# Kernel optimization log

Measured on AMD Instinct MI355X. Metric: run time of the kernel, lower is better.

## Reference

```python
import jax, jax.numpy as jnp
import numpy as np

HEADS = 16
DIM_HEAD = 64
DIM = 1024
DIM_HIDDEN = HEADS * DIM_HEAD


def setup_inputs() -> dict:
    key = jax.random.key(0)
    ks = jax.random.split(key, 5)
    b, n = 4, 2048
    x = jax.random.normal(ks[0], (b, n, DIM), dtype=jnp.float32)
    # nn.Linear weights stored as [out, in]; init ~ U(-1/sqrt(in), 1/sqrt(in))
    s = 1.0 / np.sqrt(DIM)
    w_q = jax.random.uniform(ks[1], (DIM_HIDDEN, DIM), minval=-s, maxval=s, dtype=jnp.float32)
    w_kv = jax.random.uniform(ks[2], (2 * DIM_HIDDEN, DIM), minval=-s, maxval=s, dtype=jnp.float32)
    so = 1.0 / np.sqrt(DIM_HIDDEN)
    w_out = jax.random.uniform(ks[3], (DIM, DIM_HIDDEN), minval=-so, maxval=so, dtype=jnp.float32)
    b_out = jax.random.uniform(ks[4], (DIM,), minval=-so, maxval=so, dtype=jnp.float32)
    return {"x": x, "w_q": w_q, "w_kv": w_kv, "w_out": w_out, "b_out": b_out}


def reference(x, w_q, w_kv, w_out, b_out):
    b, n, _ = x.shape
    h, e = HEADS, DIM_HEAD
    q = x @ w_q.T                     # [b, n, h*e]
    kv = x @ w_kv.T                   # [b, n, 2*h*e]
    k, v = jnp.split(kv, 2, axis=-1)
    split = lambda t: t.reshape(b, n, h, e).transpose(0, 2, 1, 3)  # [b, h, n, e]
    q, k, v = split(q), split(k), split(v)
    scale = e ** (-0.5)
    energy = jnp.einsum('bhie,bhje->bhij', q, k) * scale
    attn_w = jax.nn.softmax(energy, axis=-1)
    attn = jnp.einsum('bhij,bhje->bhie', attn_w, v)  # [b, h, n, e]
    out = attn.transpose(0, 2, 1, 3).reshape(b, n, h * e)
    return out @ w_out.T + b_out
```

## Files before the change

kernel.cpp:

```cpp
#include <hip/hip_runtime.h>

typedef __attribute__((ext_vector_type(8))) short bf16x8;
typedef __attribute__((ext_vector_type(4))) float f32x4;

#define AS1 __attribute__((address_space(1)))
#define AS3 __attribute__((address_space(3)))

#if defined(__has_builtin)
#  if __has_builtin(__builtin_amdgcn_exp2f)
#    define EXP2F(x) __builtin_amdgcn_exp2f(x)
#  endif
#endif
#ifndef EXP2F
#  define EXP2F(x) __builtin_exp2f(x)
#endif

__device__ __forceinline__ unsigned short f2bf(float f) {
    union { float f; unsigned u; } v; v.f = f;
    unsigned r = v.u + 0x7fffu + ((v.u >> 16) & 1u);
    return (unsigned short)(r >> 16);
}

__device__ __forceinline__ void dma16(const void* g, void* l) {
    __builtin_amdgcn_global_load_lds((const AS1 unsigned int*)g,
                                     (AS3 unsigned int*)l, 16, 0, 0);
}

__global__ __launch_bounds__(256) void convert_regions(
    const float* __restrict__ s0, unsigned short* __restrict__ d0, int n0, float c0,
    const float* __restrict__ s1, unsigned short* __restrict__ d1, int n1, float c1,
    const float* __restrict__ s2, unsigned short* __restrict__ d2, int n2, float c2)
{
    long long e = ((long long)blockIdx.x * 256 + threadIdx.x) * 8;
    const float* s; unsigned short* d; float sc;
    if (e < n0) { s = s0; d = d0; sc = c0; }
    else { e -= n0;
    if (e < n1) { s = s1; d = d1; sc = c1; }
    else { e -= n1;
    if (e < n2) { s = s2; d = d2; sc = c2; } else return; } }
    const float4 f0 = *(const float4*)(s + e);
    const float4 f1 = *(const float4*)(s + e + 4);
    union { unsigned short u[8]; uint4 q; } t;
    t.u[0]=f2bf(f0.x*sc); t.u[1]=f2bf(f0.y*sc); t.u[2]=f2bf(f0.z*sc); t.u[3]=f2bf(f0.w*sc);
    t.u[4]=f2bf(f1.x*sc); t.u[5]=f2bf(f1.y*sc); t.u[6]=f2bf(f1.z*sc); t.u[7]=f2bf(f1.w*sc);
    *(uint4*)(d + e) = t.q;
}

template<int CM>
__global__ __launch_bounds__(256) void gemm128(
    const unsigned short* __restrict__ A, const unsigned short* __restrict__ B,
    void* __restrict__ C0, void* __restrict__ C1, void* __restrict__ C2,
    const float* __restrict__ bias, int M, int N, int K)
{
    __shared__ __align__(16) unsigned short As[128 * 64];
    __shared__ __align__(16) unsigned short Bs[128 * 64];

    const int tid  = threadIdx.x;
    const int wq   = tid >> 6;
    const int lane = tid & 63;
    const int l16  = lane & 15;
    const int quad = lane >> 4;
    const int m0   = blockIdx.x * 128;
    const int n0   = blockIdx.y * 128;
    const int lr   = lane >> 3;
    const int cs   = lane & 7;
    const bool vswap = (CM == 1) && (n0 >= 2048);

    f32x4 acc[4][4];
#pragma unroll
    for (int mt = 0; mt < 4; ++mt)
#pragma unroll
        for (int nt = 0; nt < 4; ++nt) acc[mt][nt] = (f32x4){0.f, 0.f, 0.f, 0.f};

    for (int kk = 0; kk < K; kk += 64) {
        __syncthreads();
#pragma unroll
        for (int i = 0; i < 4; ++i) {
            const int rr = (wq * 4 + i) * 8 + lr;
            const int cg = cs ^ (rr & 7);
            dma16(A + (size_t)(m0 + rr) * K + kk + cg * 8, As + (wq * 4 + i) * 512);
            dma16(B + (size_t)(n0 + rr) * K + kk + cg * 8, Bs + (wq * 4 + i) * 512);
        }
        __syncthreads();

#pragma unroll
        for (int ch = 0; ch < 2; ++ch) {
            const int swz = (((ch * 4 + quad) ^ (l16 & 7)) * 8);
            bf16x8 aF[4], bF[4];
#pragma unroll
            for (int mt = 0; mt < 4; ++mt)
                aF[mt] = *(const bf16x8*)(As + ((wq >> 1) * 64 + mt * 16 + l16) * 64 + swz);
#pragma unroll
            for (int nt = 0; nt < 4; ++nt)
                bF[nt] = *(const bf16x8*)(Bs + ((wq & 1) * 64 + nt * 16 + l16) * 64 + swz);
            if (vswap) {
#pragma unroll
                for (int mt = 0; mt < 4; ++mt)
#pragma unroll
                    for (int nt = 0; nt < 4; ++nt)
                        acc[mt][nt] = __builtin_amdgcn_mfma_f32_16x16x32_bf16(
                            bF[nt], aF[mt], acc[mt][nt], 0, 0, 0);
            } else {
#pragma unroll
                for (int mt = 0; mt < 4; ++mt)
#pragma unroll
                    for (int nt = 0; nt < 4; ++nt)
                        acc[mt][nt] = __builtin_amdgcn_mfma_f32_16x16x32_bf16(
                            aF[mt], bF[nt], acc[mt][nt], 0, 0, 0);
            }
        }
    }

    const int wr = wq >> 1, wc = wq & 1;
    if (CM == 0) {
#pragma unroll
        for (int mt = 0; mt < 4; ++mt)
#pragma unroll
        for (int nt = 0; nt < 4; ++nt) {
            const int coln = n0 + wc * 64 + nt * 16 + l16;
            const float bv = bias ? bias[coln] : 0.f;
#pragma unroll
            for (int r = 0; r < 4; ++r) {
                const int rowm = m0 + wr * 64 + mt * 16 + quad * 4 + r;
                ((float*)C0)[(size_t)rowm * N + coln] = acc[mt][nt][r] + bv;
            }
        }
    } else if (!vswap) {
#pragma unroll
        for (int mt = 0; mt < 4; ++mt)
#pragma unroll
        for (int nt = 0; nt < 4; ++nt) {
            const int coln = n0 + wc * 64 + nt * 16 + l16;
            unsigned short* dst = (coln < 1024) ? (unsigned short*)C0 : (unsigned short*)C1;
            const int h = (coln >> 6) & 15, e = coln & 63;
#pragma unroll
            for (int r = 0; r < 4; ++r) {
                const int rowm = m0 + wr * 64 + mt * 16 + quad * 4 + r;
                const int b = rowm >> 11, n = rowm & 2047;
                dst[(((size_t)(b * 16 + h) * 2048 + n) << 6) + e] = f2bf(acc[mt][nt][r]);
            }
        }
    } else {
#pragma unroll
        for (int mt = 0; mt < 4; ++mt)
#pragma unroll
        for (int nt = 0; nt < 4; ++nt) {
#pragma unroll
            for (int r = 0; r < 4; ++r) {
                const int eg = n0 + wc * 64 + nt * 16 + quad * 4 + r;
                const int h = (eg >> 6) - 32, e = eg & 63;
                const int rowm = m0 + wr * 64 + mt * 16 + l16;
                const int b = rowm >> 11, n = rowm & 2047;
                ((unsigned short*)C2)[((size_t)(b * 16 + h) * 64 + e) * 2048 + n] =
                    f2bf(acc[mt][nt][r]);
            }
        }
    }
}

__global__ __launch_bounds__(256, 2) void attn_kernel(
    const unsigned short* __restrict__ Q, const unsigned short* __restrict__ K,
    const unsigned short* __restrict__ V, unsigned short* __restrict__ O)
{
    __shared__ __align__(16) unsigned short Ks[64 * 64];
    __shared__ __align__(16) unsigned short Vt[64 * 64];
    __shared__ __align__(16) unsigned short Ps[4 * 64 * 72];

    const int tid  = threadIdx.x;
    const int q0   = blockIdx.x * 256;
    const int bh   = blockIdx.y;
    const int wq   = tid >> 6;
    const int lane = tid & 63;
    const int l16  = lane & 15;
    const int quad = lane >> 4;
    const int lr   = lane >> 3;
    const int cs   = lane & 7;

    const unsigned short* Qg = Q + (size_t)bh * 2048 * 64;
    const unsigned short* Kg = K + (size_t)bh * 2048 * 64;
    const unsigned short* Vg = V + (size_t)bh * 64 * 2048;

    bf16x8 bQ[4][2];
#pragma unroll
    for (int sub = 0; sub < 4; ++sub)
#pragma unroll
        for (int ch = 0; ch < 2; ++ch)
            bQ[sub][ch] = *(const bf16x8*)(Qg + (size_t)(q0 + wq * 64 + sub * 16 + l16) * 64
                                           + ch * 32 + quad * 8);

    bf16x8 ones;
#pragma unroll
    for (int i = 0; i < 8; ++i) ones[i] = (short)0x3F80;

    f32x4 o[4][4], lf[4];
#pragma unroll
    for (int s = 0; s < 4; ++s) {
        lf[s] = (f32x4){0.f, 0.f, 0.f, 0.f};
#pragma unroll
        for (int e = 0; e < 4; ++e) o[s][e] = (f32x4){0.f, 0.f, 0.f, 0.f};
    }

    unsigned short* Psw = Ps + wq * 64 * 72;

    for (int kt = 0; kt < 32; ++kt) {
        const int key0 = kt * 64;
        __syncthreads();
#pragma unroll
        for (int i = 0; i < 4; ++i) {
            const int j  = wq * 4 + i;
            const int rr = (j & 7) * 8 + lr;
            const int cg = cs ^ (rr & 7);
            if (j < 8)
                dma16(Kg + (size_t)(key0 + rr) * 64 + cg * 8, Ks + (j & 7) * 512);
            else
                dma16(Vg + (size_t)rr * 2048 + key0 + cg * 8, Vt + (j & 7) * 512);
        }
        __syncthreads();

        f32x4 s[4][4];
#pragma unroll
        for (int sub = 0; sub < 4; ++sub)
#pragma unroll
            for (int c = 0; c < 4; ++c) s[sub][c] = (f32x4){0.f, 0.f, 0.f, 0.f};
#pragma unroll
        for (int ch = 0; ch < 2; ++ch) {
            const int swz = ((ch * 4 + quad) ^ (l16 & 7)) * 8;
#pragma unroll
            for (int c = 0; c < 4; ++c) {
                const bf16x8 aK = *(const bf16x8*)(Ks + (c * 16 + l16) * 64 + swz);
#pragma unroll
                for (int sub = 0; sub < 4; ++sub)
                    s[sub][c] = __builtin_amdgcn_mfma_f32_16x16x32_bf16(
                        aK, bQ[sub][ch], s[sub][c], 0, 0, 0);
            }
        }

#pragma unroll
        for (int sub = 0; sub < 4; ++sub) {
#pragma unroll
            for (int c = 0; c < 4; ++c) {
                const float p0 = EXP2F(s[sub][c][0]);
                const float p1 = EXP2F(s[sub][c][1]);
                const float p2 = EXP2F(s[sub][c][2]);
                const float p3 = EXP2F(s[sub][c][3]);
                uint2 pk;
                pk.x = __builtin_amdgcn_perm(__float_as_uint(p1), __float_as_uint(p0), 0x07060302);
                pk.y = __builtin_amdgcn_perm(__float_as_uint(p3), __float_as_uint(p2), 0x07060302);
                *(uint2*)(Psw + (sub * 16 + l16) * 72 + c * 16 + quad * 4) = pk;
            }
        }

#pragma unroll
        for (int cc = 0; cc < 2; ++cc) {
            const int swz = ((cc * 4 + quad) ^ (l16 & 7)) * 8;
            bf16x8 aP[4];
#pragma unroll
            for (int sub = 0; sub < 4; ++sub) {
                aP[sub] = *(const bf16x8*)(Psw + (sub * 16 + l16) * 72 + cc * 32 + quad * 8);
                lf[sub] = __builtin_amdgcn_mfma_f32_16x16x32_bf16(aP[sub], ones, lf[sub], 0, 0, 0);
            }
#pragma unroll
            for (int et = 0; et < 4; ++et) {
                const bf16x8 bV = *(const bf16x8*)(Vt + (et * 16 + l16) * 64 + swz);
#pragma unroll
                for (int sub = 0; sub < 4; ++sub)
                    o[sub][et] = __builtin_amdgcn_mfma_f32_16x16x32_bf16(
                        aP[sub], bV, o[sub][et], 0, 0, 0);
            }
        }
    }

    const int bb = bh >> 4, hh = bh & 15;
#pragma unroll
    for (int sub = 0; sub < 4; ++sub) {
#pragma unroll
        for (int r = 0; r < 4; ++r) {
            const float linv = 1.0f / lf[sub][r];
            const int qrow = q0 + wq * 64 + sub * 16 + quad * 4 + r;
#pragma unroll
            for (int et = 0; et < 4; ++et) {
                O[(size_t)(bb * 2048 + qrow) * 1024 + hh * 64 + et * 16 + l16] =
                    f2bf(o[sub][et][r] * linv);
            }
        }
    }
}

extern "C" void kernel_launch(void* const* d_in, const int* in_sizes, int n_in,
                              void* d_out, int out_size, void* d_ws, size_t ws_size,
                              hipStream_t stream) {
    const float* x     = (const float*)d_in[0];
    const float* w_q   = (const float*)d_in[1];
    const float* w_kv  = (const float*)d_in[2];
    const float* w_out = (const float*)d_in[3];
    const float* b_out = (const float*)d_in[4];
    const float CEXP = 0.125f * 1.44269504f;
    const size_t MB = 1024 * 1024;

    unsigned short* Qw    = (unsigned short*)d_ws;
    unsigned short* Kw    = (unsigned short*)((char*)d_ws + 16 * MB);
    unsigned short* Vw    = (unsigned short*)((char*)d_ws + 32 * MB);
    unsigned short* Ow    = (unsigned short*)((char*)d_ws + 48 * MB);
    unsigned short* xb    = (unsigned short*)d_out;
    unsigned short* wqkvb = (unsigned short*)((char*)d_out + 16 * MB);
    unsigned short* wob   = Qw;

    convert_regions<<<5632, 256, 0, stream>>>(
        x, xb, 8388608, 1.0f,
        w_q, wqkvb, 1048576, CEXP,
        w_kv, wqkvb + (size_t)1048576, 2097152, 1.0f);

    gemm128<1><<<dim3(64, 24), 256, 0, stream>>>(
        xb, wqkvb, Qw, Kw, Vw, nullptr, 8192, 3072, 1024);

    attn_kernel<<<dim3(8, 64), 256, 0, stream>>>(Qw, Kw, Vw, Ow);

    convert_regions<<<512, 256, 0, stream>>>(
        w_out, wob, 1048576, 1.0f,
        nullptr, nullptr, 0, 0.f, nullptr, nullptr, 0, 0.f);

    gemm128<0><<<dim3(64, 8), 256, 0, stream>>>(
        Ow, wob, d_out, nullptr, nullptr, b_out, 8192, 1024, 1024);
}
```

Before: 298.9 us.

## Double-buffer LDS tiles in GEMM and attention with async prefetch

Both the projection GEMM and the attention kernel now keep two LDS buffers and issue the global-to-LDS DMA for the next tile before computing on the current one. Hand-written waitcnt-plus-barrier sequences (partial vmcnt) replace the two __syncthreads per iteration, so load latency can overlap MFMA work. The cost is doubled LDS for the staging buffers, which may reduce occupancy, especially in the attention kernel. It also depends on the vmcnt values matching the number of outstanding DMA instructions.

```diff
diff --git a/kernel.cpp b/kernel.cpp
--- a/kernel.cpp
+++ b/kernel.cpp
@@ -14,6 +14,11 @@
 #ifndef EXP2F
 #  define EXP2F(x) __builtin_exp2f(x)
 #endif
+
+#define BAR_WAIT_VM8  asm volatile("s_waitcnt vmcnt(8)\ns_barrier" ::: "memory")
+#define BAR_WAIT_VM4  asm volatile("s_waitcnt vmcnt(4)\ns_barrier" ::: "memory")
+#define BAR_WAIT_VM0  asm volatile("s_waitcnt vmcnt(0)\ns_barrier" ::: "memory")
+#define BAR_WAIT_LGKM asm volatile("s_waitcnt lgkmcnt(0)\ns_barrier" ::: "memory")
 
 __device__ __forceinline__ unsigned short f2bf(float f) {
     union { float f; unsigned u; } v; v.f = f;
@@ -52,8 +57,7 @@
     void* __restrict__ C0, void* __restrict__ C1, void* __restrict__ C2,
     const float* __restrict__ bias, int M, int N, int K)
 {
-    __shared__ __align__(16) unsigned short As[128 * 64];
-    __shared__ __align__(16) unsigned short Bs[128 * 64];
+    __shared__ __align__(16) unsigned short smem[2 * 16384];
 
     const int tid  = threadIdx.x;
     const int wq   = tid >> 6;
@@ -72,27 +76,41 @@
 #pragma unroll
         for (int nt = 0; nt < 4; ++nt) acc[mt][nt] = (f32x4){0.f, 0.f, 0.f, 0.f};
 
-    for (int kk = 0; kk < K; kk += 64) {
-        __syncthreads();
+    auto issue = [&](int buf, int kk) {
+        unsigned short* as = smem + buf * 16384;
+        unsigned short* bs = as + 8192;
 #pragma unroll
         for (int i = 0; i < 4; ++i) {
             const int rr = (wq * 4 + i) * 8 + lr;
             const int cg = cs ^ (rr & 7);
-            dma16(A + (size_t)(m0 + rr) * K + kk + cg * 8, As + (wq * 4 + i) * 512);
-            dma16(B + (size_t)(n0 + rr) * K + kk + cg * 8, Bs + (wq * 4 + i) * 512);
-        }
-        __syncthreads();
-
+            dma16(A + (size_t)(m0 + rr) * K + kk + cg * 8, as + (wq * 4 + i) * 512);
+            dma16(B + (size_t)(n0 + rr) * K + kk + cg * 8, bs + (wq * 4 + i) * 512);
+        }
+    };
+
+    const int nIt = K >> 6;
+    issue(0, 0);
+#pragma unroll 2
+    for (int it = 0; it < nIt; ++it) {
+        const int cur = it & 1;
+        if (it + 1 < nIt) {
+            issue(cur ^ 1, (it + 1) << 6);
+            BAR_WAIT_VM8;
+        } else {
+            BAR_WAIT_VM0;
+        }
+        const unsigned short* as = smem + cur * 16384;
+        const unsigned short* bs = as + 8192;
 #pragma unroll
         for (int ch = 0; ch < 2; ++ch) {
             const int swz = (((ch * 4 + quad) ^ (l16 & 7)) * 8);
             bf16x8 aF[4], bF[4];
 #pragma unroll
             for (int mt = 0; mt < 4; ++mt)
-                aF[mt] = *(const bf16x8*)(As + ((wq >> 1) * 64 + mt * 16 + l16) * 64 + swz);
+                aF[mt] = *(const bf16x8*)(as + ((wq >> 1) * 64 + mt * 16 + l16) * 64 + swz);
 #pragma unroll
             for (int nt = 0; nt < 4; ++nt)
-                bF[nt] = *(const bf16x8*)(Bs + ((wq & 1) * 64 + nt * 16 + l16) * 64 + swz);
+                bF[nt] = *(const bf16x8*)(bs + ((wq & 1) * 64 + nt * 16 + l16) * 64 + swz);
             if (vswap) {
 #pragma unroll
                 for (int mt = 0; mt < 4; ++mt)
@@ -109,6 +127,7 @@
                             aF[mt], bF[nt], acc[mt][nt], 0, 0, 0);
             }
         }
+        BAR_WAIT_LGKM;
     }
 
     const int wr = wq >> 1, wc = wq & 1;
@@ -162,8 +181,7 @@
     const unsigned short* __restrict__ Q, const unsigned short* __restrict__ K,
     const unsigned short* __restrict__ V, unsigned short* __restrict__ O)
 {
-    __shared__ __align__(16) unsigned short Ks[64 * 64];
-    __shared__ __align__(16) unsigned short Vt[64 * 64];
+    __shared__ __align__(16) unsigned short KVs[2 * 8192];
     __shared__ __align__(16) unsigned short Ps[4 * 64 * 72];
 
     const int tid  = threadIdx.x;
@@ -202,20 +220,33 @@
 
     unsigned short* Psw = Ps + wq * 64 * 72;
 
-    for (int kt = 0; kt < 32; ++kt) {
-        const int key0 = kt * 64;
-        __syncthreads();
+    auto issueKV = [&](int buf, int key0) {
+        unsigned short* ks = KVs + buf * 8192;
+        unsigned short* vt = ks + 4096;
 #pragma unroll
         for (int i = 0; i < 4; ++i) {
             const int j  = wq * 4 + i;
             const int rr = (j & 7) * 8 + lr;
             const int cg = cs ^ (rr & 7);
             if (j < 8)
-                dma16(Kg + (size_t)(key0 + rr) * 64 + cg * 8, Ks + (j & 7) * 512);
+                dma16(Kg + (size_t)(key0 + rr) * 64 + cg * 8, ks + (j & 7) * 512);
             else
-                dma16(Vg + (size_t)rr * 2048 + key0 + cg * 8, Vt + (j & 7) * 512);
-        }
-        __syncthreads();
+                dma16(Vg + (size_t)rr * 2048 + key0 + cg * 8, vt + (j & 7) * 512);
+        }
+    };
+
+    issueKV(0, 0);
+#pragma unroll 2
+    for (int kt = 0; kt < 32; ++kt) {
+        const int cur = kt & 1;
+        if (kt + 1 < 32) {
+            issueKV(cur ^ 1, (kt + 1) * 64);
+            BAR_WAIT_VM4;
+        } else {
+            BAR_WAIT_VM0;
+        }
+        const unsigned short* ks = KVs + cur * 8192;
+        const unsigned short* vt = ks + 4096;
 
         f32x4 s[4][4];
 #pragma unroll
@@ -227,7 +258,7 @@
             const int swz = ((ch * 4 + quad) ^ (l16 & 7)) * 8;
 #pragma unroll
             for (int c = 0; c < 4; ++c) {
-                const bf16x8 aK = *(const bf16x8*)(Ks + (c * 16 + l16) * 64 + swz);
+                const bf16x8 aK = *(const bf16x8*)(ks + (c * 16 + l16) * 64 + swz);
 #pragma unroll
                 for (int sub = 0; sub < 4; ++sub)
                     s[sub][c] = __builtin_amdgcn_mfma_f32_16x16x32_bf16(
@@ -261,13 +292,14 @@
             }
 #pragma unroll
             for (int et = 0; et < 4; ++et) {
-                const bf16x8 bV = *(const bf16x8*)(Vt + (et * 16 + l16) * 64 + swz);
+                const bf16x8 bV = *(const bf16x8*)(vt + (et * 16 + l16) * 64 + swz);
 #pragma unroll
                 for (int sub = 0; sub < 4; ++sub)
                     o[sub][et] = __builtin_amdgcn_mfma_f32_16x16x32_bf16(
                         aP[sub], bV, o[sub][et], 0, 0, 0);
             }
         }
+        BAR_WAIT_LGKM;
     }
 
     const int bb = bh >> 4, hh = bh & 15;
```

After: 248.1 us. 1.2x faster.
